# Optimization experiments

Measured on AMD Instinct MI355X. Metric: run time of the kernel, lower is better.

## Reference

```python
import jax, jax.numpy as jnp
import numpy as np

WINDOW = 14
NUM_HEADS = 12
DIM = 768
HEAD_DIM = DIM // NUM_HEADS
SCALE = HEAD_DIM ** (-0.5)


def _relative_position_index(ws):
    coords = np.stack(np.meshgrid(np.arange(ws), np.arange(ws), indexing='ij'))  # [2, ws, ws]
    flat = coords.reshape(2, -1)  # [2, ws*ws]
    rel = flat[:, :, None] - flat[:, None, :]  # [2, N, N]
    rel = rel.transpose(1, 2, 0)  # [N, N, 2]
    rel[:, :, 0] += ws - 1
    rel[:, :, 1] += ws - 1
    rel[:, :, 0] *= 2 * ws - 1
    return rel.sum(-1).astype(np.int32)  # [N, N]


def setup_inputs() -> dict:
    key = jax.random.key(0)
    ks = jax.random.split(key, 7)
    B, N = 64, WINDOW * WINDOW
    x = jax.random.normal(ks[0], (B, N, DIM), dtype=jnp.float32)
    qkv_weight = jax.random.normal(ks[1], (3 * DIM, DIM), dtype=jnp.float32) * 0.02
    q_bias = jax.random.normal(ks[2], (DIM,), dtype=jnp.float32) * 0.02
    v_bias = jax.random.normal(ks[3], (DIM,), dtype=jnp.float32) * 0.02
    rpb_table = jax.random.normal(ks[4], ((2 * WINDOW - 1) ** 2, NUM_HEADS), dtype=jnp.float32) * 0.02
    rel_pos_index = jnp.asarray(_relative_position_index(WINDOW))
    proj_weight = jax.random.normal(ks[5], (DIM, DIM), dtype=jnp.float32) * 0.02
    proj_bias = jax.random.normal(ks[6], (DIM,), dtype=jnp.float32) * 0.02
    return {"x": x, "qkv_weight": qkv_weight, "q_bias": q_bias, "v_bias": v_bias,
            "rpb_table": rpb_table, "rel_pos_index": rel_pos_index,
            "proj_weight": proj_weight, "proj_bias": proj_bias}


def reference(x, qkv_weight, q_bias, v_bias, rpb_table, rel_pos_index, proj_weight, proj_bias):
    B, N, C = x.shape
    H, hd = NUM_HEADS, HEAD_DIM
    # qkv bias = [q_bias, zeros, v_bias]
    qkv_bias = jnp.concatenate([q_bias, jnp.zeros_like(v_bias), v_bias])
    qkv = x @ qkv_weight.T + qkv_bias  # [B, N, 3C]
    qkv = qkv.reshape(B, N, 3, H, hd).transpose(2, 0, 3, 1, 4)  # [3, B, H, N, hd]
    q, k, v = qkv[0], qkv[1], qkv[2]
    attn = jnp.einsum('bhnd,bhmd->bhnm', q * SCALE, k)  # [B, H, N, N]
    # relative position bias: gather [N*N, H] -> [H, N, N]
    rpb = rpb_table[rel_pos_index.reshape(-1)].reshape(N, N, H).transpose(2, 0, 1)
    attn = jax.nn.softmax(attn + rpb[None], axis=-1)
    out = jnp.einsum('bhnm,bhmd->bhnd', attn, v)  # [B, H, N, hd]
    out = out.transpose(0, 2, 1, 3).reshape(B, N, H * hd)
    return out @ proj_weight.T + proj_bias
```

## Files before the change

### kernel.cpp

```cpp
#include <hip/hip_runtime.h>
#include <hip/hip_bf16.h>
#include <stdint.h>

typedef __attribute__((ext_vector_type(8))) short bf16x8_t;
typedef __attribute__((ext_vector_type(4))) float f32x4_t;
typedef unsigned int u32;
typedef unsigned short u16;
typedef u32 __attribute__((address_space(3))) lds_u32;
typedef u32 __attribute__((address_space(1))) gbl_u32;

#define NUM_H 12
#define NTOK 196
#define NBATCH 64
#define CDIM 768
#define VTS 224
#define VLS 232
#define RPS 208

__device__ __forceinline__ u16 f2bf(float f) {
    u32 u = __float_as_uint(f);
    u32 r = u + 0x7FFFu + ((u >> 16) & 1u);
    return (u16)(r >> 16);
}

__global__ void cvt_kernel(const float* __restrict__ in, u16* __restrict__ out, int n) {
    int n4 = n >> 2;
    for (int i = blockIdx.x * blockDim.x + threadIdx.x; i < n4; i += gridDim.x * blockDim.x) {
        float4 v = ((const float4*)in)[i];
        ushort4 o;
        o.x = f2bf(v.x); o.y = f2bf(v.y); o.z = f2bf(v.z); o.w = f2bf(v.w);
        ((ushort4*)out)[i] = o;
    }
}

__global__ void rpb_kernel(const float* __restrict__ table, const int* __restrict__ idx,
                           float* __restrict__ rpbt) {
    int ij = blockIdx.x * 256 + threadIdx.x;
    if (ij < NTOK * NTOK) {
        const int qr = ij / NTOK, col = ij - qr * NTOK;
        const int rp = idx[ij];
        #pragma unroll
        for (int h = 0; h < NUM_H; h++)
            rpbt[((size_t)h * RPS + col) * RPS + qr] = table[rp * NUM_H + h];
    }
}

__global__ __launch_bounds__(256, 3) void gemm_kernel(
    const u16* __restrict__ A, const u16* __restrict__ W, int K, int mode,
    const float* __restrict__ bias_q, const float* __restrict__ bias_v,
    u16* __restrict__ oq, u16* __restrict__ ok, u16* __restrict__ ovt,
    const float* __restrict__ pbias, float* __restrict__ of) {
    __shared__ __align__(16) u16 lds[3][2][4096];
    const int tid = threadIdx.x;
    const int wave = tid >> 6, lane = tid & 63;
    const int wr = wave >> 1, wc = wave & 1;
    const int bid = blockIdx.x;
    const int xcd = bid & 7, i = bid >> 3;
    const int i13 = i / 13;
    const int bm = xcd * 13 + (i - i13 * 13);
    const int bn = i13;
    if (bm >= 98) return;

    f32x4_t acc[4][4];
    #pragma unroll
    for (int ii = 0; ii < 4; ii++)
        #pragma unroll
        for (int jj = 0; jj < 4; jj++) acc[ii][jj] = f32x4_t{0.f, 0.f, 0.f, 0.f};

    auto stage = [&](int buf, int kt) {
        const int k0 = kt * 32;
        const int su = (lane & 3) ^ ((lane >> 2) & 3);
        #pragma unroll
        for (int c2 = 0; c2 < 2; c2++) {
            const int c = wave * 2 + c2;
            {
                const int row = bm * 128 + c * 16 + (lane >> 2);
                const u16* src = A + (size_t)row * K + k0 + su * 8;
                __builtin_amdgcn_global_load_lds((gbl_u32*)src, (lds_u32*)&lds[buf][0][c * 512], 16, 0, 0);
            }
            {
                const int row = bn * 128 + c * 16 + (lane >> 2);
                const u16* src = W + (size_t)row * K + k0 + su * 8;
                __builtin_amdgcn_global_load_lds((gbl_u32*)src, (lds_u32*)&lds[buf][1][c * 512], 16, 0, 0);
            }
        }
    };

    const int NKT = K >> 5;
    stage(0, 0);
    if (NKT > 1) stage(1, 1);
    for (int kt = 0; kt < NKT; ++kt) {
        const int buf = kt % 3;
        if (kt + 1 < NKT) {
            asm volatile("s_waitcnt vmcnt(4)" ::: "memory");
        } else {
            asm volatile("s_waitcnt vmcnt(0)" ::: "memory");
        }
        __builtin_amdgcn_s_barrier();
        if (kt + 2 < NKT) stage((kt + 2) % 3, kt + 2);
        bf16x8_t af[4], bfr[4];
        #pragma unroll
        for (int mt = 0; mt < 4; mt++) {
            const int r = wr * 64 + mt * 16 + (lane & 15);
            const int u = (lane >> 4) ^ (r & 3);
            af[mt] = *(const bf16x8_t*)&lds[buf][0][r * 32 + u * 8];
        }
        #pragma unroll
        for (int nt = 0; nt < 4; nt++) {
            const int r = wc * 64 + nt * 16 + (lane & 15);
            const int u = (lane >> 4) ^ (r & 3);
            bfr[nt] = *(const bf16x8_t*)&lds[buf][1][r * 32 + u * 8];
        }
        __builtin_amdgcn_s_setprio(1);
        #pragma unroll
        for (int mt = 0; mt < 4; mt++)
            #pragma unroll
            for (int nt = 0; nt < 4; nt++)
                acc[mt][nt] = __builtin_amdgcn_mfma_f32_16x16x32_bf16(af[mt], bfr[nt], acc[mt][nt], 0, 0, 0);
        __builtin_amdgcn_s_setprio(0);
    }

    const int g = lane >> 4;
    if (mode == 0) {
        #pragma unroll
        for (int nt = 0; nt < 4; nt++) {
            const int n = bn * 128 + wc * 64 + nt * 16 + (lane & 15);
            const int which = n / CDIM;
            const int rem = n - which * CDIM;
            const int hh = rem >> 6, d = rem & 63;
            const float bias = (which == 0) ? bias_q[rem] : (which == 2 ? bias_v[rem] : 0.f);
            #pragma unroll
            for (int mt = 0; mt < 4; mt++) {
                const int m0 = bm * 128 + wr * 64 + mt * 16 + 4 * g;
                const int bb = m0 / NTOK, t0 = m0 - bb * NTOK;
                if (which == 2) {
                    ushort4 vv;
                    vv.x = f2bf(acc[mt][nt][0] + bias);
                    vv.y = f2bf(acc[mt][nt][1] + bias);
                    vv.z = f2bf(acc[mt][nt][2] + bias);
                    vv.w = f2bf(acc[mt][nt][3] + bias);
                    *(ushort4*)&ovt[(((size_t)bb * NUM_H + hh) * 64 + d) * VTS + t0] = vv;
                } else {
                    u16* dst = (which == 0) ? oq : ok;
                    #pragma unroll
                    for (int r = 0; r < 4; r++) {
                        float v = acc[mt][nt][r] + bias;
                        if (which == 0) v *= 0.125f;
                        dst[(((size_t)bb * NUM_H + hh) * NTOK + t0 + r) * 64 + d] = f2bf(v);
                    }
                }
            }
        }
    } else {
        #pragma unroll
        for (int mt = 0; mt < 4; mt++) {
            #pragma unroll
            for (int r = 0; r < 4; r++) {
                const int m = bm * 128 + wr * 64 + mt * 16 + 4 * g + r;
                #pragma unroll
                for (int nt = 0; nt < 4; nt++) {
                    const int n = bn * 128 + wc * 64 + nt * 16 + (lane & 15);
                    of[(size_t)m * CDIM + n] = acc[mt][nt][r] + pbias[n];
                }
            }
        }
    }
}

__global__ __launch_bounds__(256, 2) void attn_kernel(
    const u16* __restrict__ Q, const u16* __restrict__ Kg, const u16* __restrict__ Vt,
    const float* __restrict__ rpbt, u16* __restrict__ O) {
    __shared__ __align__(16) u16 Ks[208 * 64];
    __shared__ __align__(16) u16 Vs[64 * VLS];
    __shared__ __align__(16) u16 Ps[4][16 * 64];
    const int lane = threadIdx.x & 63, wave = threadIdx.x >> 6;
    const int bh = (blockIdx.x & 7) + 8 * (blockIdx.x >> 3);
    const int b = bh / NUM_H, h = bh - b * NUM_H;
    const u16* Qb = Q + (size_t)bh * NTOK * 64;
    const u16* Kb = Kg + (size_t)bh * NTOK * 64;
    const u16* Vgb = Vt + (size_t)bh * 64 * VTS;
    const int g = lane >> 4, lc = lane & 15;

    for (int c = wave; c < 26 + 29; c += 4) {
        if (c < 26) {
            const int row = c * 8 + (lane >> 3);
            const int u = lane & 7;
            const int srow = (row < NTOK) ? row : (NTOK - 1);
            const u16* src = Kb + srow * 64 + ((u ^ (row & 7)) << 3);
            __builtin_amdgcn_global_load_lds((gbl_u32*)src, (lds_u32*)&Ks[c * 512], 16, 0, 0);
        } else {
            const int p = (c - 26) * 1024 + lane * 16;
            const int d = p / (VLS * 2);
            const int off = p - d * (VLS * 2);
            const u16* src = (off < VTS * 2) ? (Vgb + d * VTS + (off >> 1)) : Vgb;
            __builtin_amdgcn_global_load_lds((gbl_u32*)src, (lds_u32*)((char*)Vs + (c - 26) * 1024), 16, 0, 0);
        }
    }
    if (wave == 2) asm volatile("s_waitcnt vmcnt(8)" ::: "memory");
    else           asm volatile("s_waitcnt vmcnt(7)" ::: "memory");
    __builtin_amdgcn_s_barrier();

    bool vpending = true;
    for (int qt = wave; qt < 13; qt += 4) {
        const float* rpbc = rpbt + ((size_t)h * RPS + lc) * RPS + qt * 16 + 4 * g;
        bf16x8_t qf[2];
        const int qrow_f = qt * 16 + lc;
        #pragma unroll
        for (int kk = 0; kk < 2; kk++) {
            if (qrow_f < NTOK) qf[kk] = *(const bf16x8_t*)(Qb + qrow_f * 64 + kk * 32 + g * 8);
            else qf[kk] = bf16x8_t{0, 0, 0, 0, 0, 0, 0, 0};
        }
        float4 rp13[13];
        #pragma unroll
        for (int nt = 0; nt < 13; nt++) rp13[nt] = *(const float4*)(rpbc + nt * 16 * RPS);
        f32x4_t s[13];
        #pragma unroll
        for (int nt = 0; nt < 13; nt++) s[nt] = f32x4_t{0.f, 0.f, 0.f, 0.f};
        #pragma unroll
        for (int nt = 0; nt < 13; nt++) {
            #pragma unroll
            for (int kk = 0; kk < 2; kk++) {
                const int kr = nt * 16 + lc;
                const int u = (kk * 4 + g) ^ (kr & 7);
                bf16x8_t kf = *(const bf16x8_t*)&Ks[kr * 64 + u * 8];
                s[nt] = __builtin_amdgcn_mfma_f32_16x16x32_bf16(qf[kk], kf, s[nt], 0, 0, 0);
            }
        }
        float mx[4] = {-3e38f, -3e38f, -3e38f, -3e38f};
        #pragma unroll
        for (int nt = 0; nt < 13; nt++) {
            const int col = nt * 16 + lc;
            const float rpv[4] = {rp13[nt].x, rp13[nt].y, rp13[nt].z, rp13[nt].w};
            #pragma unroll
            for (int r = 0; r < 4; r++) {
                const int qr = qt * 16 + 4 * g + r;
                float v;
                if (col < NTOK && qr < NTOK) v = s[nt][r] + rpv[r];
                else v = -1e30f;
                s[nt][r] = v;
                mx[r] = fmaxf(mx[r], v);
            }
        }
        #pragma unroll
        for (int r = 0; r < 4; r++) {
            mx[r] = fmaxf(mx[r], __shfl_xor(mx[r], 1));
            mx[r] = fmaxf(mx[r], __shfl_xor(mx[r], 2));
            mx[r] = fmaxf(mx[r], __shfl_xor(mx[r], 4));
            mx[r] = fmaxf(mx[r], __shfl_xor(mx[r], 8));
        }
        float sm[4] = {0.f, 0.f, 0.f, 0.f};
        #pragma unroll
        for (int nt = 0; nt < 13; nt++)
            #pragma unroll
            for (int r = 0; r < 4; r++) {
                float p = __expf(s[nt][r] - mx[r]);
                s[nt][r] = p;
                sm[r] += p;
            }
        float inv[4];
        #pragma unroll
        for (int r = 0; r < 4; r++) {
            sm[r] += __shfl_xor(sm[r], 1);
            sm[r] += __shfl_xor(sm[r], 2);
            sm[r] += __shfl_xor(sm[r], 4);
            sm[r] += __shfl_xor(sm[r], 8);
            inv[r] = 1.f / sm[r];
        }

        if (vpending) {
            asm volatile("s_waitcnt vmcnt(0)" ::: "memory");
            __builtin_amdgcn_s_barrier();
            vpending = false;
        }

        f32x4_t o4[4];
        #pragma unroll
        for (int dt = 0; dt < 4; dt++) o4[dt] = f32x4_t{0.f, 0.f, 0.f, 0.f};
        for (int kc = 0; kc < 4; kc++) {
            #pragma unroll
            for (int ntl = 0; ntl < 4; ntl++) {
                const int nt = kc * 4 + ntl;
                const int kl = ntl * 16 + lc;
                #pragma unroll
                for (int r = 0; r < 4; r++) {
                    const int rr = 4 * g + r;
                    u16 pv = 0;
                    if (nt < 13) pv = f2bf(s[nt][r]);
                    Ps[wave][rr * 64 + (((kl >> 3) ^ (rr & 7)) << 3) + (kl & 7)] = pv;
                }
            }
            asm volatile("s_waitcnt lgkmcnt(0)" ::: "memory");
            const int nsteps = (kc < 3) ? 2 : 1;
            for (int ks = 0; ks < nsteps; ks++) {
                const int rr = lc;
                const int u = (ks * 4 + g) ^ (rr & 7);
                bf16x8_t pf = *(const bf16x8_t*)&Ps[wave][rr * 64 + u * 8];
                #pragma unroll
                for (int dt = 0; dt < 4; dt++) {
                    const int dcol = dt * 16 + lc;
                    const int kb = kc * 64 + ks * 32 + g * 8;
                    bf16x8_t vf = *(const bf16x8_t*)&Vs[dcol * VLS + kb];
                    o4[dt] = __builtin_amdgcn_mfma_f32_16x16x32_bf16(pf, vf, o4[dt], 0, 0, 0);
                }
            }
            asm volatile("" ::: "memory");
        }
        #pragma unroll
        for (int dt = 0; dt < 4; dt++)
            #pragma unroll
            for (int r = 0; r < 4; r++) {
                const int qr = qt * 16 + 4 * g + r;
                if (qr < NTOK)
                    O[((size_t)b * NTOK + qr) * CDIM + h * 64 + dt * 16 + lc] = f2bf(o4[dt][r] * inv[r]);
            }
    }
}

extern "C" void kernel_launch(void* const* d_in, const int* in_sizes, int n_in,
                              void* d_out, int out_size, void* d_ws, size_t ws_size,
                              hipStream_t stream) {
    const float* x = (const float*)d_in[0];
    const float* qkvw = (const float*)d_in[1];
    const float* qb = (const float*)d_in[2];
    const float* vb = (const float*)d_in[3];
    const float* rpbt = (const float*)d_in[4];
    const int* rpi = (const int*)d_in[5];
    const float* pw = (const float*)d_in[6];
    const float* pb = (const float*)d_in[7];
    float* out = (float*)d_out;

    char* ws = (char*)d_ws;
    size_t off = 0;
    auto alloc = [&](size_t bytes) {
        void* p = ws + off;
        off += (bytes + 255) & ~(size_t)255;
        return p;
    };
    const size_t MROWS = 12544;
    u16* xbf = (u16*)alloc(MROWS * 768 * 2);
    u16* wbf = (u16*)alloc((size_t)2304 * 768 * 2);
    u16* pwbf = (u16*)alloc((size_t)768 * 768 * 2);
    u16* qws = (u16*)alloc(MROWS * 768 * 2);
    u16* kws = (u16*)alloc(MROWS * 768 * 2);
    u16* vtws = (u16*)alloc((size_t)768 * 64 * VTS * 2 + 256);
    u16* aout = (u16*)alloc(MROWS * 768 * 2);
    float* rpbm = (float*)alloc((size_t)NUM_H * RPS * RPS * 4 + 256);

    cvt_kernel<<<2048, 256, 0, stream>>>(x, xbf, 12544 * 768);
    cvt_kernel<<<1024, 256, 0, stream>>>(qkvw, wbf, 2304 * 768);
    cvt_kernel<<<512, 256, 0, stream>>>(pw, pwbf, 768 * 768);
    rpb_kernel<<<(196 * 196 + 255) / 256, 256, 0, stream>>>(rpbt, rpi, rpbm);
    gemm_kernel<<<8 * 13 * 18, 256, 0, stream>>>(xbf, wbf, 768, 0, qb, vb, qws, kws, vtws, nullptr, nullptr);
    attn_kernel<<<768, 256, 0, stream>>>(qws, kws, vtws, rpbm, aout);
    gemm_kernel<<<8 * 13 * 6, 256, 0, stream>>>(aout, pwbf, 768, 1, nullptr, nullptr, nullptr, nullptr, nullptr, pb, out);
}
```

Measured before the change: 159.1 us.

## Fuse conversion launches, widen LDS swizzle, stage Q/K epilogue through LDS

Measured after the change: 153.9 us. 3.2% less time.

```diff
diff --git a/kernel.cpp b/kernel.cpp
--- a/kernel.cpp
+++ b/kernel.cpp
@@ -23,13 +23,21 @@
     return (u16)(r >> 16);
 }
 
-__global__ void cvt_kernel(const float* __restrict__ in, u16* __restrict__ out, int n) {
-    int n4 = n >> 2;
-    for (int i = blockIdx.x * blockDim.x + threadIdx.x; i < n4; i += gridDim.x * blockDim.x) {
-        float4 v = ((const float4*)in)[i];
+__global__ void cvt3_kernel(const float* __restrict__ a, u16* __restrict__ oa, int na4,
+                            const float* __restrict__ b, u16* __restrict__ ob, int nb4,
+                            const float* __restrict__ c, u16* __restrict__ oc, int nc4) {
+    const int total = na4 + nb4 + nc4;
+    for (int i = blockIdx.x * blockDim.x + threadIdx.x; i < total; i += gridDim.x * blockDim.x) {
+        const float* src;
+        u16* dst;
+        int j = i;
+        if (j < na4) { src = a; dst = oa; }
+        else if ((j -= na4) < nb4) { src = b; dst = ob; }
+        else { j -= nb4; src = c; dst = oc; }
+        float4 v = ((const float4*)src)[j];
         ushort4 o;
         o.x = f2bf(v.x); o.y = f2bf(v.y); o.z = f2bf(v.z); o.w = f2bf(v.w);
-        ((ushort4*)out)[i] = o;
+        ((ushort4*)dst)[j] = o;
     }
 }
 
@@ -69,7 +77,7 @@
 
     auto stage = [&](int buf, int kt) {
         const int k0 = kt * 32;
-        const int su = (lane & 3) ^ ((lane >> 2) & 3);
+        const int su = (lane & 3) ^ ((lane >> 2) & 3) ^ ((lane >> 4) & 3);
         #pragma unroll
         for (int c2 = 0; c2 < 2; c2++) {
             const int c = wave * 2 + c2;
@@ -102,13 +110,13 @@
         #pragma unroll
         for (int mt = 0; mt < 4; mt++) {
             const int r = wr * 64 + mt * 16 + (lane & 15);
-            const int u = (lane >> 4) ^ (r & 3);
+            const int u = (lane >> 4) ^ (r & 3) ^ ((r >> 2) & 3);
             af[mt] = *(const bf16x8_t*)&lds[buf][0][r * 32 + u * 8];
         }
         #pragma unroll
         for (int nt = 0; nt < 4; nt++) {
             const int r = wc * 64 + nt * 16 + (lane & 15);
-            const int u = (lane >> 4) ^ (r & 3);
+            const int u = (lane >> 4) ^ (r & 3) ^ ((r >> 2) & 3);
             bfr[nt] = *(const bf16x8_t*)&lds[buf][1][r * 32 + u * 8];
         }
         __builtin_amdgcn_s_setprio(1);
@@ -120,35 +128,59 @@
         __builtin_amdgcn_s_setprio(0);
     }
 
-    const int g = lane >> 4;
+    const int g = lane >> 4, lc = lane & 15;
     if (mode == 0) {
-        #pragma unroll
-        for (int nt = 0; nt < 4; nt++) {
-            const int n = bn * 128 + wc * 64 + nt * 16 + (lane & 15);
-            const int which = n / CDIM;
-            const int rem = n - which * CDIM;
-            const int hh = rem >> 6, d = rem & 63;
-            const float bias = (which == 0) ? bias_q[rem] : (which == 2 ? bias_v[rem] : 0.f);
-            #pragma unroll
-            for (int mt = 0; mt < 4; mt++) {
-                const int m0 = bm * 128 + wr * 64 + mt * 16 + 4 * g;
-                const int bb = m0 / NTOK, t0 = m0 - bb * NTOK;
-                if (which == 2) {
+        const int n_base = bn * 128 + wc * 64;
+        const int which = n_base / CDIM;
+        const int rem0 = n_base - which * CDIM;
+        if (which == 2) {
+            #pragma unroll
+            for (int nt = 0; nt < 4; nt++) {
+                const int rem = rem0 + nt * 16 + lc;
+                const int hh = rem >> 6, d = rem & 63;
+                const float bias = bias_v[rem];
+                #pragma unroll
+                for (int mt = 0; mt < 4; mt++) {
+                    const int m0 = bm * 128 + wr * 64 + mt * 16 + 4 * g;
+                    const int bb = m0 / NTOK, t0 = m0 - bb * NTOK;
                     ushort4 vv;
                     vv.x = f2bf(acc[mt][nt][0] + bias);
                     vv.y = f2bf(acc[mt][nt][1] + bias);
                     vv.z = f2bf(acc[mt][nt][2] + bias);
                     vv.w = f2bf(acc[mt][nt][3] + bias);
                     *(ushort4*)&ovt[(((size_t)bb * NUM_H + hh) * 64 + d) * VTS + t0] = vv;
-                } else {
-                    u16* dst = (which == 0) ? oq : ok;
+                }
+            }
+        } else {
+            u16* tile = ((u16*)lds) + wave * 4096;
+            const float scale = (which == 0) ? 0.125f : 1.f;
+            #pragma unroll
+            for (int nt = 0; nt < 4; nt++) {
+                const int rem = rem0 + nt * 16 + lc;
+                const float bias = (which == 0) ? bias_q[rem] : 0.f;
+                const int nl = nt * 16 + lc;
+                #pragma unroll
+                for (int mt = 0; mt < 4; mt++) {
                     #pragma unroll
                     for (int r = 0; r < 4; r++) {
-                        float v = acc[mt][nt][r] + bias;
-                        if (which == 0) v *= 0.125f;
-                        dst[(((size_t)bb * NUM_H + hh) * NTOK + t0 + r) * 64 + d] = f2bf(v);
+                        const int ml = mt * 16 + 4 * g + r;
+                        const int nsw = (nl & 7) | ((((nl >> 3) ^ (ml & 7)) & 7) << 3);
+                        tile[ml * 64 + nsw] = f2bf((acc[mt][nt][r] + bias) * scale);
                     }
                 }
+            }
+            asm volatile("s_waitcnt lgkmcnt(0)" ::: "memory");
+            u16* dst = (which == 0) ? oq : ok;
+            const int hh = rem0 >> 6;
+            #pragma unroll
+            for (int it = 0; it < 8; it++) {
+                const int ml = it * 8 + (lane >> 3);
+                const int u = lane & 7;
+                const int usw = u ^ (ml & 7);
+                bf16x8_t v = *(const bf16x8_t*)&tile[ml * 64 + usw * 8];
+                const int mg = bm * 128 + wr * 64 + ml;
+                const int bb = mg / NTOK, t = mg - bb * NTOK;
+                *(bf16x8_t*)&dst[(((size_t)bb * NUM_H + hh) * NTOK + t) * 64 + u * 8] = v;
             }
         }
     } else {
@@ -159,7 +191,7 @@
                 const int m = bm * 128 + wr * 64 + mt * 16 + 4 * g + r;
                 #pragma unroll
                 for (int nt = 0; nt < 4; nt++) {
-                    const int n = bn * 128 + wc * 64 + nt * 16 + (lane & 15);
+                    const int n = bn * 128 + wc * 64 + nt * 16 + lc;
                     of[(size_t)m * CDIM + n] = acc[mt][nt][r] + pbias[n];
                 }
             }
@@ -346,9 +378,9 @@
     u16* aout = (u16*)alloc(MROWS * 768 * 2);
     float* rpbm = (float*)alloc((size_t)NUM_H * RPS * RPS * 4 + 256);
 
-    cvt_kernel<<<2048, 256, 0, stream>>>(x, xbf, 12544 * 768);
-    cvt_kernel<<<1024, 256, 0, stream>>>(qkvw, wbf, 2304 * 768);
-    cvt_kernel<<<512, 256, 0, stream>>>(pw, pwbf, 768 * 768);
+    cvt3_kernel<<<2048, 256, 0, stream>>>(x, xbf, (12544 * 768) / 4,
+                                          qkvw, wbf, (2304 * 768) / 4,
+                                          pw, pwbf, (768 * 768) / 4);
     rpb_kernel<<<(196 * 196 + 255) / 256, 256, 0, stream>>>(rpbt, rpi, rpbm);
     gemm_kernel<<<8 * 13 * 18, 256, 0, stream>>>(xbf, wbf, 768, 0, qb, vb, qws, kws, vtws, nullptr, nullptr);
     attn_kernel<<<768, 256, 0, stream>>>(qws, kws, vtws, rpbm, aout);
```
